# Kernel optimization log

Measured on AMD Instinct MI355X. Metric: run time of the kernel, lower is better.

## Reference

```python
import jax, jax.numpy as jnp
import numpy as np
from jax.scipy.special import logsumexp

B, T, F = 32, 256, 32   # batch, line width (time), line height (features)
HID = 128
VOCAB = 100             # blank index = VOCAB
LBL = 32                # label length
NEG = -1e30


def _mdlstm(x, Wx, Wh1, Wh2, b):
    # x: [B, H, W, C] -> 2D LSTM: outer scan over width, inner scan over height
    Bb, H, W, C = x.shape
    hid = Wh1.shape[0]

    def col_step(carry, x_col):
        c_left, h_left = carry  # [H, B, hid] states from previous column

        def row_step(rc, inp):
            c_up, h_up = rc          # [B, hid] from previous row
            x_ij, c_l, h_l = inp     # [B, C], [B, hid], [B, hid]
            z = x_ij @ Wx + h_l @ Wh1 + h_up @ Wh2 + b  # [B, 5*hid]
            i_, g_, f1, f2, o_ = jnp.split(z, 5, axis=-1)
            c = jax.nn.sigmoid(f1) * c_l + jax.nn.sigmoid(f2) * c_up + jax.nn.sigmoid(i_) * jnp.tanh(g_)
            h = jax.nn.sigmoid(o_) * jnp.tanh(c)
            return (c, h), (c, h)

        z0 = jnp.zeros((Bb, hid), x.dtype)
        _, (c_col, h_col) = jax.lax.scan(row_step, (z0, z0), (x_col, c_left, h_left))
        return (c_col, h_col), h_col

    x_t = jnp.transpose(x, (2, 1, 0, 3))  # [W, H, B, C]
    zc = jnp.zeros((H, Bb, hid), x.dtype)
    _, hs = jax.lax.scan(col_step, (zc, zc), x_t)  # [W, H, B, hid]
    return jnp.transpose(hs, (2, 1, 0, 3))  # [B, H, W, hid]


def _ctc_loss(logp, labels, blank):
    # logp: [B, T, V] log-softmax; labels: [B, L] int in [0, blank)
    Bb, Tt, V = logp.shape
    Ll = labels.shape[1]
    S = 2 * Ll + 1
    ext = jnp.full((Bb, S), blank, dtype=labels.dtype).at[:, 1::2].set(labels)  # blank-interleaved
    lp_ext = jnp.take_along_axis(logp, jnp.broadcast_to(ext[:, None, :], (Bb, Tt, S)), axis=2)  # [B,T,S]
    prev2 = jnp.concatenate([jnp.full((Bb, 2), blank, dtype=ext.dtype), ext[:, :-2]], axis=1)
    skip = (ext != blank) & (ext != prev2)
    skip = skip.at[:, :2].set(False)
    alpha0 = jnp.full((Bb, S), NEG, logp.dtype).at[:, 0].set(lp_ext[:, 0, 0]).at[:, 1].set(lp_ext[:, 0, 1])

    def step(alpha, lp_t):
        a1 = jnp.concatenate([jnp.full((Bb, 1), NEG, alpha.dtype), alpha[:, :-1]], axis=1)
        a2 = jnp.concatenate([jnp.full((Bb, 2), NEG, alpha.dtype), alpha[:, :-2]], axis=1)
        a2 = jnp.where(skip, a2, NEG)
        new = logsumexp(jnp.stack([alpha, a1, a2], axis=0), axis=0) + lp_t
        return new, None

    alphaT, _ = jax.lax.scan(step, alpha0, jnp.transpose(lp_ext, (1, 0, 2))[1:])
    ll = logsumexp(jnp.stack([alphaT[:, -1], alphaT[:, -2]], axis=0), axis=0)
    return -ll  # [B]


def setup_inputs() -> dict:
    key = jax.random.key(0)
    ks = jax.random.split(key, 8)
    s = 0.08
    return {
        "X": jax.random.normal(ks[0], (B, T, F), jnp.float32),
        "y": jax.random.randint(ks[1], (B, LBL), 0, VOCAB),
        "Wx": jax.random.normal(ks[2], (1, 5 * HID), jnp.float32) * s,
        "Wh1": jax.random.normal(ks[3], (HID, 5 * HID), jnp.float32) * s,
        "Wh2": jax.random.normal(ks[4], (HID, 5 * HID), jnp.float32) * s,
        "b": jax.random.normal(ks[5], (5 * HID,), jnp.float32) * 0.01,
        "W_fc": jax.random.normal(ks[6], (HID, VOCAB + 1), jnp.float32) * s,
        "b_fc": jax.random.normal(ks[7], (VOCAB + 1,), jnp.float32) * 0.01,
    }


def reference(X, y, Wx, Wh1, Wh2, b, W_fc, b_fc):
    x = jnp.transpose(X, (0, 2, 1))[..., None]        # [B, F, T, 1] (image)
    h = _mdlstm(x, Wx, Wh1, Wh2, b)                    # [B, F, T, HID]
    feat = jnp.sum(h, axis=1)                          # collapse over height -> [B, T, HID]
    logits = feat @ W_fc + b_fc                        # [B, T, VOCAB+1]
    logp = jax.nn.log_softmax(logits, axis=-1)
    return _ctc_loss(logp, y, VOCAB)                   # per-example CTC loss [B]
```

## Files before the change

kernel.cpp:

```cpp
#include <hip/hip_runtime.h>

#define NEGF (-1e30f)

typedef __attribute__((ext_vector_type(8))) short short8;
typedef __attribute__((ext_vector_type(4))) float float4v;

template <bool V> struct BC { static constexpr bool value = V; };

__device__ __forceinline__ short f2bf(float f) {
  union { float f; unsigned u; } v; v.f = f;
  unsigned r = v.u + 0x7fffu + ((v.u >> 16) & 1u);
  return (short)(r >> 16);
}
__device__ __forceinline__ float fastrcp(float x) { return __builtin_amdgcn_rcpf(x); }
__device__ __forceinline__ float clamp15(float x) { return fminf(15.0f, fmaxf(-15.0f, x)); }

__global__ void prep_w_kernel(const float* __restrict__ Wh1, const float* __restrict__ Wh2,
                              short* __restrict__ wsW) {
  int t = blockIdx.x * 256 + threadIdx.x;
  int lane = t & 63;
  int frag = t >> 6;
  int nt = frag >> 3, kk = frag & 7;
  int n  = nt * 16 + (lane & 15);
  int kb = kk * 32 + (lane >> 4) * 8;
  short8 v;
#pragma unroll
  for (int j = 0; j < 8; ++j) {
    int k = kb + j;
    float w = (k < 128) ? Wh1[k * 640 + n] : Wh2[(k - 128) * 640 + n];
    v[j] = f2bf(w);
  }
  ((short8*)wsW)[frag * 64 + lane] = v;
}

__global__ __launch_bounds__(512)
void mdlstm_kernel(const float* __restrict__ X, const short* __restrict__ wsW,
                   const float* __restrict__ Wx, const float* __restrict__ bias,
                   float* __restrict__ feat, float* __restrict__ bH0,
                   float* __restrict__ bC0, int* __restrict__ flagA,
                   int* __restrict__ flagB) {
  __shared__ __align__(16) short h_buf[2][17][136];
  __shared__ __align__(16) short wlds[128 * 512];
  __shared__ float featbuf[17][132];

  const int blk  = blockIdx.x;
  const int bat  = blk >> 1;
  const bool isB = blk & 1;
  const int tid  = threadIdx.x;
  const int lane = tid & 63;
  const int g    = tid >> 6;
  const int col  = lane & 15;
  const int quad = lane >> 4;
  const int jj   = g * 16 + col;

  for (int i = tid; i < 2 * 17 * 136 / 2; i += 512) ((int*)h_buf)[i] = 0;
  for (int i = tid; i < 17 * 132; i += 512) ((float*)featbuf)[i] = 0.0f;
  {
    const uint4* src = (const uint4*)(wsW + 192 * 512);
    uint4* dst = (uint4*)wlds;
    for (int i = tid; i < 8192; i += 512) dst[i] = src[i];
  }

  float wx[5], bg[5];
#pragma unroll
  for (int q = 0; q < 5; ++q) {
    wx[q] = Wx[q * 128 + jj];
    bg[q] = bias[q * 128 + jj];
  }
  float cp[4] = {0.f, 0.f, 0.f, 0.f};
  float c15 = 0.0f;
  float pre_h = 0.0f, pre_c = 0.0f;
  int knownA = 0;

  const float* Xg = X + bat * 8192;
  float* fb = feat + bat * 32768;
  float* bH = bH0 + bat * 32 * 128;
  float* bC = bC0 + bat * 32 * 128;
  int* fA = flagA + bat;
  int* fB = flagB + bat;
  const short8* W8 = (const short8*)wsW;
  const short8* pW0 = W8 + ((0 * 8 + g) * 8) * 64 + lane;
  const short8* pW1 = W8 + ((1 * 8 + g) * 8) * 64 + lane;
  const short8* pW2 = W8 + ((2 * 8 + g) * 8) * 64 + lane;
  const short8* pL3 = (const short8*)&wlds[((0 * 8 + g) * 8) * 512 + lane * 8];
  const short8* pL4 = (const short8*)&wlds[((1 * 8 + g) * 8) * 512 + lane * 8];
  const int mbase = (isB ? 16 : 0) + quad * 4;
  const int widx0 = (isB ? 1 : 0) + quad * 4;
  const float* pX = Xg - 31 * mbase;
  int sb = 0;
  __syncthreads();

  auto step = [&](int d, auto isb_, auto allv_) {
    constexpr bool IsB = decltype(isb_)::value;
    constexpr bool ALLV = decltype(allv_)::value;
    const int rbuf = (d + 1) & 1, wbuf = d & 1;

    const int wfl = d - (IsB ? 32 : 16);
    if (wfl >= 0 && tid < 128) {
      int fs = sb + 1; if (fs >= 17) fs = 0;
      float v = featbuf[fs][tid];
      featbuf[fs][tid] = 0.0f;
      atomicAdd(&fb[wfl * 128 + tid], v);
    }

    float4v acc[5];
#pragma unroll
    for (int q = 0; q < 5; ++q) acc[q] = (float4v){bg[q], bg[q], bg[q], bg[q]};
    const short8 z8 = (short8){0, 0, 0, 0, 0, 0, 0, 0};
#pragma unroll
    for (int kk = 0; kk < 8; ++kk) {
      const int up = (kk >= 4) ? 1 : 0;
      const int cc = (kk & 3) * 32 + quad * 8;
      int row = col + (IsB ? 1 : 0) - up;
      short8 a0 = (IsB || row >= 0) ? *(const short8*)&h_buf[rbuf][row][cc] : z8;
      short8 b3 = pL3[kk * 64];
      acc[3] = __builtin_amdgcn_mfma_f32_16x16x32_bf16(a0, b3, acc[3], 0, 0, 0);
      short8 b4 = pL4[kk * 64];
      acc[4] = __builtin_amdgcn_mfma_f32_16x16x32_bf16(a0, b4, acc[4], 0, 0, 0);
      short8 b2 = pW2[kk * 64];
      acc[2] = __builtin_amdgcn_mfma_f32_16x16x32_bf16(a0, b2, acc[2], 0, 0, 0);
      short8 b0 = pW0[kk * 64];
      acc[0] = __builtin_amdgcn_mfma_f32_16x16x32_bf16(a0, b0, acc[0], 0, 0, 0);
      short8 b1 = pW1[kk * 64];
      acc[1] = __builtin_amdgcn_mfma_f32_16x16x32_bf16(a0, b1, acc[1], 0, 0, 0);
    }

    float t0 = __shfl_up(cp[3], 16);
    float cu[4];
    cu[0] = quad ? t0 : (IsB ? c15 : 0.0f);
    cu[1] = cp[0]; cu[2] = cp[1]; cu[3] = cp[2];
    const float* pXd = pX + d * 32;
    float xm[4];
#pragma unroll
    for (int r = 0; r < 4; ++r) {
      int w = d - (mbase + r);
      if (ALLV || (w >= 0 && w < 256)) xm[r] = pXd[-31 * r];
    }
#pragma unroll
    for (int r = 0; r < 4; ++r) {
      const int w = d - (mbase + r);
      if (ALLV || (w >= 0 && w < 256)) {
        float c_up = cu[r];
        float c_l  = cp[r];
        float x    = xm[r];
        float zi = clamp15(fmaf(x, wx[0], acc[0][r]));
        float zg = clamp15(fmaf(x, wx[1], acc[1][r]));
        float z1 = clamp15(fmaf(x, wx[2], acc[2][r]));
        float z2 = clamp15(fmaf(x, wx[3], acc[3][r]));
        float zo = clamp15(fmaf(x, wx[4], acc[4][r]));
        float e1 = __expf(z1), e2 = __expf(z2), ei = __expf(zi), eg = __expf(2.0f * zg);
        float A1 = 1.0f + e1, A2 = 1.0f + e2, Ai = 1.0f + ei, G = 1.0f + eg;
        float P = Ai * G, Q = A1 * A2;
        float rD = fastrcp(P * Q);
        float c = (e1 * c_l * (A2 * P) + e2 * c_up * (A1 * P) + ei * (eg - 1.0f) * Q) * rD;
        float eo = __expf(-zo);
        float ec = __expf(2.0f * clamp15(c));
        float h = (ec - 1.0f) * fastrcp((1.0f + eo) * (ec + 1.0f));
        cp[r] = c;
        h_buf[wbuf][widx0 + r][jj] = f2bf(h);
        int s = sb - (quad * 4 + r); if (s < 0) s += 17;
        featbuf[s][jj] += h;
        if (!IsB && r == 3 && quad == 3 && d >= 15) {
          const int slot = (d & 31) * 128 + jj;
          atomicExch(&bH[slot], h);
          atomicExch(&bC[slot], c);
        }
      }
    }
  };

  BC<true> Tv; BC<false> Fv;
  if (!isB) {
    auto aiter = [&](int d, auto allv) {
      if (d >= 48 && (d & 7) == 0 && lane == 0) {
        while (atomicAdd(fB, 0) < d - 22) {}
      }
      step(d, Fv, allv);
      sb = (sb == 16) ? 0 : sb + 1;
      __syncthreads();
      if ((((d + 1) & 7) == 0 || d == 270) && tid == 0) atomicExch(fA, d + 1);
    };
    for (int d = 0; d < 15; ++d)    aiter(d, Fv);
    for (int d = 15; d < 256; ++d)  aiter(d, Tv);
    for (int d = 256; d < 271; ++d) aiter(d, Fv);
    if (tid < 128) atomicAdd(&fb[255 * 128 + tid], featbuf[0][tid]);
  } else {
    {
      if (lane == 0) { while (atomicAdd(fA, 0) < 23) {} knownA = 23; }
      const int slot = 15 * 128 + jj;
      if (quad == 1) pre_h = atomicAdd(&bH[slot], 0.0f);
      else if (quad == 0) pre_c = atomicAdd(&bC[slot], 0.0f);
    }
    auto biter = [&](int e, auto allv) {
      if (quad == 1) h_buf[(e + 1) & 1][0][jj] = f2bf(pre_h);
      else if (quad == 0) c15 = pre_c;
      const int ee = e + 1;
      if (ee <= 271) {
        if (lane == 0 && knownA < ee) {
          int tgt = ee + 7; if (tgt > 271) tgt = 271;
          while (atomicAdd(fA, 0) < tgt) {}
          knownA = tgt;
        }
        const int slot = ((ee - 1) & 31) * 128 + jj;
        if (quad == 1) pre_h = atomicAdd(&bH[slot], 0.0f);
        else if (quad == 0) pre_c = atomicAdd(&bC[slot], 0.0f);
      } else {
        pre_h = 0.0f; pre_c = 0.0f;
      }
      __syncthreads();
      step(e, Tv, allv);
      sb = (sb == 16) ? 0 : sb + 1;
      if (((e & 7) == 7 || e == 286) && tid == 0) atomicExch(fB, e);
    };
    for (int e = 16; e < 31; ++e)   biter(e, Fv);
    for (int e = 31; e < 272; ++e)  biter(e, Tv);
    for (int e = 272; e < 287; ++e) biter(e, Fv);
    __syncthreads();
    if (tid < 128) atomicAdd(&fb[255 * 128 + tid], featbuf[0][tid]);
  }
}

__global__ __launch_bounds__(256)
void logits_kernel(const float* __restrict__ feat, const float* __restrict__ Wfc,
                   const float* __restrict__ bfc, float* __restrict__ logp) {
  __shared__ float sW[128 * 101];
  __shared__ float sF[8][128];
  __shared__ float sL[8][104];
  __shared__ float sLse[8];
  const int tid = threadIdx.x;
  const int b  = blockIdx.x >> 5;
  const int t0 = (blockIdx.x & 31) * 8;

  for (int i = tid; i < 128 * 101; i += 256) sW[i] = Wfc[i];
  for (int i = tid; i < 8 * 128; i += 256)
    sF[i >> 7][i & 127] = feat[(b * 256 + t0 + (i >> 7)) * 128 + (i & 127)];
  __syncthreads();
  for (int idx = tid; idx < 8 * 101; idx += 256) {
    int tr = idx / 101, v = idx - tr * 101;
    float s = bfc[v];
#pragma unroll 4
    for (int k = 0; k < 128; ++k) s += sF[tr][k] * sW[k * 101 + v];
    sL[tr][v] = s;
  }
  __syncthreads();
  if (tid < 8) {
    float m = NEGF;
    for (int v = 0; v < 101; ++v) m = fmaxf(m, sL[tid][v]);
    float su = 0.0f;
    for (int v = 0; v < 101; ++v) su += __expf(sL[tid][v] - m);
    sLse[tid] = m + __logf(su);
  }
  __syncthreads();
  for (int idx = tid; idx < 8 * 101; idx += 256) {
    int tr = idx / 101, v = idx - tr * 101;
    logp[(b * 256 + t0 + tr) * 101 + v] = sL[tr][v] - sLse[tr];
  }
}

__global__ __launch_bounds__(64)
void ctc_kernel(const float* __restrict__ logp, const int* __restrict__ y,
                float* __restrict__ out) {
  const int b = blockIdx.x;
  const int l = threadIdx.x;
  const float* lpb = logp + b * 256 * 101;
  const int* yb = y + b * 32;
  int lab = (l & 1) ? yb[l >> 1] : 100;
  bool skip = (l & 1) && (l >= 3) && (yb[l >> 1] != yb[(l >> 1) - 1]);

  float a   = (l == 0) ? lpb[100] : ((l == 1) ? lpb[lab] : NEGF);
  float a64 = NEGF;
  float pl[4], pb[4];
#pragma unroll
  for (int tt = 0; tt < 4; ++tt) {
    pl[tt] = lpb[(1 + tt) * 101 + lab];
    pb[tt] = lpb[(1 + tt) * 101 + 100];
  }
#pragma unroll 4
  for (int t = 1; t < 256; ++t) {
    const int s = (t - 1) & 3;
    float lpl = pl[s], lpbk = pb[s];
    if (t + 4 < 256) {
      pl[s] = lpb[(t + 4) * 101 + lab];
      pb[s] = lpb[(t + 4) * 101 + 100];
    }
    float am1 = __shfl_up(a, 1); if (l == 0) am1 = NEGF;
    float am2 = __shfl_up(a, 2); if (l < 2 || !skip) am2 = NEGF;
    float m3 = fmaxf(a, fmaxf(am1, am2));
    float na = m3 + __logf(__expf(a - m3) + __expf(am1 - m3) + __expf(am2 - m3)) + lpl;
    float m2 = fmaxf(a64, a);
    float na64 = m2 + __logf(__expf(a64 - m2) + __expf(a - m2)) + lpbk;
    a = na;
    a64 = na64;
  }
  float A63 = __shfl(a, 63);
  float A64 = __shfl(a64, 63);
  if (l == 0) {
    float m = fmaxf(A63, A64);
    out[b] = -(m + __logf(__expf(A63 - m) + __expf(A64 - m)));
  }
}

extern "C" void kernel_launch(void* const* d_in, const int* in_sizes, int n_in,
                              void* d_out, int out_size, void* d_ws, size_t ws_size,
                              hipStream_t stream) {
  const float* X   = (const float*)d_in[0];
  const int*   y   = (const int*)d_in[1];
  const float* Wx  = (const float*)d_in[2];
  const float* Wh1 = (const float*)d_in[3];
  const float* Wh2 = (const float*)d_in[4];
  const float* bi  = (const float*)d_in[5];
  const float* Wfc = (const float*)d_in[6];
  const float* bfc = (const float*)d_in[7];
  float* out = (float*)d_out;

  char* ws = (char*)d_ws;
  short* wsW  = (short*)(ws);
  float* bndH = (float*)(ws + 0x50000);
  float* bndC = (float*)(ws + 0xD0000);
  int*   flgA = (int*)(ws + 0x150000);
  int*   flgB = (int*)(ws + 0x150800);
  float* logp = (float*)(ws + 0x50000);
  float* feat = (float*)(ws + 0x378000);

  hipMemsetAsync(feat, 0, 32 * 256 * 128 * sizeof(float), stream);
  prep_w_kernel<<<80, 256, 0, stream>>>(Wh1, Wh2, wsW);
  mdlstm_kernel<<<64, 512, 0, stream>>>(X, wsW, Wx, bi, feat, bndH, bndC, flgA, flgB);
  logits_kernel<<<1024, 256, 0, stream>>>(feat, Wfc, bfc, logp);
  ctc_kernel<<<32, 64, 0, stream>>>(logp, y, out);
}
```

Measured before the change: 866.3 us.

## Fuse logits and CTC epilogues into the MDLSTM kernel using the paired blocks

Folds the logits/log-softmax and CTC stages into the tail of the MDLSTM kernel. Each of the two blocks per batch computes logits for half the time steps in place in the feature buffer, with flag handshakes so each half is only read once it is complete, and block B then runs the CTC recursion. This removes two kernel launches and the separate logp round trip, and block B's progress flag is published before each step instead of after. The cost is that the CTC tail now runs on only 32 blocks and adds extra spin-wait synchronisation between paired blocks. Also swaps the clamp for a single fmed3 instruction.

```diff
diff --git a/kernel.cpp b/kernel.cpp
--- a/kernel.cpp
+++ b/kernel.cpp
@@ -13,7 +13,7 @@
   return (short)(r >> 16);
 }
 __device__ __forceinline__ float fastrcp(float x) { return __builtin_amdgcn_rcpf(x); }
-__device__ __forceinline__ float clamp15(float x) { return fminf(15.0f, fmaxf(-15.0f, x)); }
+__device__ __forceinline__ float clamp15(float x) { return __builtin_amdgcn_fmed3f(x, -15.0f, 15.0f); }
 
 __global__ void prep_w_kernel(const float* __restrict__ Wh1, const float* __restrict__ Wh2,
                               short* __restrict__ wsW) {
@@ -38,10 +38,13 @@
                    const float* __restrict__ Wx, const float* __restrict__ bias,
                    float* __restrict__ feat, float* __restrict__ bH0,
                    float* __restrict__ bC0, int* __restrict__ flagA,
-                   int* __restrict__ flagB) {
+                   int* __restrict__ flagB, const float* __restrict__ Wfc,
+                   const float* __restrict__ bfc, const int* __restrict__ y,
+                   float* __restrict__ out) {
   __shared__ __align__(16) short h_buf[2][17][136];
   __shared__ __align__(16) short wlds[128 * 512];
   __shared__ float featbuf[17][132];
+  __shared__ float sF[8][128];
 
   const int blk  = blockIdx.x;
   const int bat  = blk >> 1;
@@ -169,6 +172,45 @@
     }
   };
 
+  auto logits_ep = [&](int base) {
+    float* sW = (float*)wlds;
+    for (int i = tid; i < 128 * 101; i += 512) sW[i] = Wfc[i];
+    __syncthreads();
+    for (int tile = 0; tile < 16; ++tile) {
+      const int t0 = base + tile * 8;
+      for (int i = tid; i < 1024; i += 512) {
+        int r = i >> 7, k = i & 127;
+        sF[r][k] = __hip_atomic_load(&fb[(t0 + r) * 128 + k], __ATOMIC_RELAXED,
+                                     __HIP_MEMORY_SCOPE_AGENT);
+      }
+      __syncthreads();
+      const int r = g;
+      float s0 = bfc[lane];
+#pragma unroll 8
+      for (int k = 0; k < 128; ++k) s0 = fmaf(sF[r][k], sW[k * 101 + lane], s0);
+      float s1 = NEGF;
+      if (lane + 64 < 101) {
+        float t = bfc[lane + 64];
+#pragma unroll 8
+        for (int k = 0; k < 128; ++k) t = fmaf(sF[r][k], sW[k * 101 + lane + 64], t);
+        s1 = t;
+      }
+      float mx = fmaxf(s0, s1);
+#pragma unroll
+      for (int off = 32; off; off >>= 1) mx = fmaxf(mx, __shfl_xor(mx, off));
+      float su = __expf(s0 - mx) + __expf(s1 - mx);
+#pragma unroll
+      for (int off = 32; off; off >>= 1) su += __shfl_xor(su, off);
+      float lse = mx + __logf(su);
+      __hip_atomic_store(&fb[(t0 + r) * 128 + lane], s0 - lse, __ATOMIC_RELAXED,
+                         __HIP_MEMORY_SCOPE_AGENT);
+      if (lane + 64 < 101)
+        __hip_atomic_store(&fb[(t0 + r) * 128 + lane + 64], s1 - lse, __ATOMIC_RELAXED,
+                           __HIP_MEMORY_SCOPE_AGENT);
+      __syncthreads();
+    }
+  };
+
   BC<true> Tv; BC<false> Fv;
   if (!isB) {
     auto aiter = [&](int d, auto allv) {
@@ -184,6 +226,13 @@
     for (int d = 15; d < 256; ++d)  aiter(d, Tv);
     for (int d = 256; d < 271; ++d) aiter(d, Fv);
     if (tid < 128) atomicAdd(&fb[255 * 128 + tid], featbuf[0][tid]);
+    __syncthreads();
+    if (tid == 0) atomicExch(fA, 272);
+    if (lane == 0) { while (atomicAdd(fB, 0) < 159) {} }
+    __syncthreads();
+    logits_ep(0);
+    __syncthreads();
+    if (tid == 0) atomicExch(fA, 273);
   } else {
     {
       if (lane == 0) { while (atomicAdd(fA, 0) < 23) {} knownA = 23; }
@@ -208,95 +257,64 @@
         pre_h = 0.0f; pre_c = 0.0f;
       }
       __syncthreads();
+      if ((e & 7) == 0 && e >= 24 && tid == 0) atomicExch(fB, e - 1);
       step(e, Tv, allv);
       sb = (sb == 16) ? 0 : sb + 1;
-      if (((e & 7) == 7 || e == 286) && tid == 0) atomicExch(fB, e);
     };
     for (int e = 16; e < 31; ++e)   biter(e, Fv);
     for (int e = 31; e < 272; ++e)  biter(e, Tv);
     for (int e = 272; e < 287; ++e) biter(e, Fv);
     __syncthreads();
     if (tid < 128) atomicAdd(&fb[255 * 128 + tid], featbuf[0][tid]);
-  }
-}
-
-__global__ __launch_bounds__(256)
-void logits_kernel(const float* __restrict__ feat, const float* __restrict__ Wfc,
-                   const float* __restrict__ bfc, float* __restrict__ logp) {
-  __shared__ float sW[128 * 101];
-  __shared__ float sF[8][128];
-  __shared__ float sL[8][104];
-  __shared__ float sLse[8];
-  const int tid = threadIdx.x;
-  const int b  = blockIdx.x >> 5;
-  const int t0 = (blockIdx.x & 31) * 8;
-
-  for (int i = tid; i < 128 * 101; i += 256) sW[i] = Wfc[i];
-  for (int i = tid; i < 8 * 128; i += 256)
-    sF[i >> 7][i & 127] = feat[(b * 256 + t0 + (i >> 7)) * 128 + (i & 127)];
-  __syncthreads();
-  for (int idx = tid; idx < 8 * 101; idx += 256) {
-    int tr = idx / 101, v = idx - tr * 101;
-    float s = bfc[v];
+    __syncthreads();
+    if (lane == 0) { while (atomicAdd(fA, 0) < 272) {} }
+    __syncthreads();
+    logits_ep(128);
+    __syncthreads();
+    if (lane == 0) { while (atomicAdd(fA, 0) < 273) {} }
+    __syncthreads();
+
+    if (tid < 64) {
+      const int l = tid;
+      const int* yb = y + bat * 32;
+      int lab = (l & 1) ? yb[l >> 1] : 100;
+      bool skip = (l & 1) && (l >= 3) && (yb[l >> 1] != yb[(l >> 1) - 1]);
+      auto LP = [&](int t, int v) {
+        return __hip_atomic_load(&fb[t * 128 + v], __ATOMIC_RELAXED,
+                                 __HIP_MEMORY_SCOPE_AGENT);
+      };
+      float a   = (l == 0) ? LP(0, 100) : ((l == 1) ? LP(0, lab) : NEGF);
+      float a64 = NEGF;
+      float pl[4], pb[4];
+#pragma unroll
+      for (int tt = 0; tt < 4; ++tt) {
+        pl[tt] = LP(1 + tt, lab);
+        pb[tt] = LP(1 + tt, 100);
+      }
 #pragma unroll 4
-    for (int k = 0; k < 128; ++k) s += sF[tr][k] * sW[k * 101 + v];
-    sL[tr][v] = s;
-  }
-  __syncthreads();
-  if (tid < 8) {
-    float m = NEGF;
-    for (int v = 0; v < 101; ++v) m = fmaxf(m, sL[tid][v]);
-    float su = 0.0f;
-    for (int v = 0; v < 101; ++v) su += __expf(sL[tid][v] - m);
-    sLse[tid] = m + __logf(su);
-  }
-  __syncthreads();
-  for (int idx = tid; idx < 8 * 101; idx += 256) {
-    int tr = idx / 101, v = idx - tr * 101;
-    logp[(b * 256 + t0 + tr) * 101 + v] = sL[tr][v] - sLse[tr];
-  }
-}
-
-__global__ __launch_bounds__(64)
-void ctc_kernel(const float* __restrict__ logp, const int* __restrict__ y,
-                float* __restrict__ out) {
-  const int b = blockIdx.x;
-  const int l = threadIdx.x;
-  const float* lpb = logp + b * 256 * 101;
-  const int* yb = y + b * 32;
-  int lab = (l & 1) ? yb[l >> 1] : 100;
-  bool skip = (l & 1) && (l >= 3) && (yb[l >> 1] != yb[(l >> 1) - 1]);
-
-  float a   = (l == 0) ? lpb[100] : ((l == 1) ? lpb[lab] : NEGF);
-  float a64 = NEGF;
-  float pl[4], pb[4];
-#pragma unroll
-  for (int tt = 0; tt < 4; ++tt) {
-    pl[tt] = lpb[(1 + tt) * 101 + lab];
-    pb[tt] = lpb[(1 + tt) * 101 + 100];
-  }
-#pragma unroll 4
-  for (int t = 1; t < 256; ++t) {
-    const int s = (t - 1) & 3;
-    float lpl = pl[s], lpbk = pb[s];
-    if (t + 4 < 256) {
-      pl[s] = lpb[(t + 4) * 101 + lab];
-      pb[s] = lpb[(t + 4) * 101 + 100];
-    }
-    float am1 = __shfl_up(a, 1); if (l == 0) am1 = NEGF;
-    float am2 = __shfl_up(a, 2); if (l < 2 || !skip) am2 = NEGF;
-    float m3 = fmaxf(a, fmaxf(am1, am2));
-    float na = m3 + __logf(__expf(a - m3) + __expf(am1 - m3) + __expf(am2 - m3)) + lpl;
-    float m2 = fmaxf(a64, a);
-    float na64 = m2 + __logf(__expf(a64 - m2) + __expf(a - m2)) + lpbk;
-    a = na;
-    a64 = na64;
-  }
-  float A63 = __shfl(a, 63);
-  float A64 = __shfl(a64, 63);
-  if (l == 0) {
-    float m = fmaxf(A63, A64);
-    out[b] = -(m + __logf(__expf(A63 - m) + __expf(A64 - m)));
+      for (int t = 1; t < 256; ++t) {
+        const int s = (t - 1) & 3;
+        float lpl = pl[s], lpbk = pb[s];
+        if (t + 4 < 256) {
+          pl[s] = LP(t + 4, lab);
+          pb[s] = LP(t + 4, 100);
+        }
+        float am1 = __shfl_up(a, 1); if (l == 0) am1 = NEGF;
+        float am2 = __shfl_up(a, 2); if (l < 2 || !skip) am2 = NEGF;
+        float m3 = fmaxf(a, fmaxf(am1, am2));
+        float na = m3 + __logf(__expf(a - m3) + __expf(am1 - m3) + __expf(am2 - m3)) + lpl;
+        float m2 = fmaxf(a64, a);
+        float na64 = m2 + __logf(__expf(a64 - m2) + __expf(a - m2)) + lpbk;
+        a = na;
+        a64 = na64;
+      }
+      float A63 = __shfl(a, 63);
+      float A64 = __shfl(a64, 63);
+      if (l == 0) {
+        float m = fmaxf(A63, A64);
+        out[bat] = -(m + __logf(__expf(A63 - m) + __expf(A64 - m)));
+      }
+    }
   }
 }
 
@@ -319,12 +337,10 @@
   float* bndC = (float*)(ws + 0xD0000);
   int*   flgA = (int*)(ws + 0x150000);
   int*   flgB = (int*)(ws + 0x150800);
-  float* logp = (float*)(ws + 0x50000);
   float* feat = (float*)(ws + 0x378000);
 
   hipMemsetAsync(feat, 0, 32 * 256 * 128 * sizeof(float), stream);
   prep_w_kernel<<<80, 256, 0, stream>>>(Wh1, Wh2, wsW);
-  mdlstm_kernel<<<64, 512, 0, stream>>>(X, wsW, Wx, bi, feat, bndH, bndC, flgA, flgB);
-  logits_kernel<<<1024, 256, 0, stream>>>(feat, Wfc, bfc, logp);
-  ctc_kernel<<<32, 64, 0, stream>>>(logp, y, out);
+  mdlstm_kernel<<<64, 512, 0, stream>>>(X, wsW, Wx, bi, feat, bndH, bndC, flgA, flgB,
+                                        Wfc, bfc, y, out);
 }
```

After: 912.6 us. +5.3%, slower.
